# Kernel optimization log

Measured on AMD Instinct MI355X. Metric: run time of the kernel, lower is better.

Reference implementation:

```python
import jax, jax.numpy as jnp
import numpy as np

B, N, C, H, L, D_FF = 32, 196, 768, 12, 4, 3072

def _ln(x, g, b, eps=1e-6):
    m = x.mean(-1, keepdims=True)
    v = ((x - m) ** 2).mean(-1, keepdims=True)
    return (x - m) / jnp.sqrt(v + eps) * g + b

def _sdpa(q, k, v, scale):
    a = jax.nn.softmax(jnp.einsum('...qd,...kd->...qk', q, k) * scale, axis=-1)
    return jnp.einsum('...qk,...kd->...qd', a, v)

def _vit_attn(x, qkv_w, qkv_b, proj_w, proj_b):
    Bs, Ns, Cs = x.shape
    hd = Cs // H
    qkv = (x @ qkv_w + qkv_b).reshape(Bs, Ns, 3, H, hd).transpose(2, 0, 3, 1, 4)
    q, k, v = qkv[0], qkv[1], qkv[2]  # [B,H,N,hd]
    o = _sdpa(q, k, v, hd ** -0.5).transpose(0, 2, 1, 3).reshape(Bs, Ns, Cs)
    return o @ proj_w + proj_b

def _mlp(x, w1, b1, w2, b2):
    return jax.nn.gelu(x @ w1 + b1, approximate=False) @ w2 + b2

def setup_inputs() -> dict:
    key = jax.random.key(0)
    ks = jax.random.split(key, 16)
    w = lambda k, s: (jax.random.normal(k, s, jnp.float32) * 0.02)
    inp = {
        'x': jax.random.normal(ks[0], (B, N, C), jnp.float32),
        'y': jax.random.normal(ks[1], (B, N, C), jnp.float32),
        'latents': w(ks[2], (1, L, C)),
        'scale_a': jnp.zeros((1,), jnp.float32),
        'scale_v': jnp.zeros((1,), jnp.float32),
    }
    for i, p in enumerate(['s', 'r']):
        kk = jax.random.split(ks[3 + i], 4)
        inp.update({
            f'{p}_ln1_g': jnp.ones((C,), jnp.float32),
            f'{p}_ln1_b': jnp.zeros((C,), jnp.float32),
            f'{p}_qkv_w': w(kk[0], (C, 3 * C)),
            f'{p}_qkv_b': jnp.zeros((3 * C,), jnp.float32),
            f'{p}_proj_w': w(kk[1], (C, C)),
            f'{p}_proj_b': jnp.zeros((C,), jnp.float32),
            f'{p}_ln2_g': jnp.ones((C,), jnp.float32),
            f'{p}_ln2_b': jnp.zeros((C,), jnp.float32),
            f'{p}_fc1_w': w(kk[2], (C, D_FF)),
            f'{p}_fc1_b': jnp.zeros((D_FF,), jnp.float32),
            f'{p}_fc2_w': w(kk[3], (D_FF, C)),
            f'{p}_fc2_b': jnp.zeros((C,), jnp.float32),
        })
    return inp

def reference(x, y, latents, scale_a, scale_v,
              s_ln1_g, s_ln1_b, s_qkv_w, s_qkv_b, s_proj_w, s_proj_b,
              s_ln2_g, s_ln2_b, s_fc1_w, s_fc1_b, s_fc2_w, s_fc2_b,
              r_ln1_g, r_ln1_b, r_qkv_w, r_qkv_b, r_proj_w, r_proj_b,
              r_ln2_g, r_ln2_b, r_fc1_w, r_fc1_b, r_fc2_w, r_fc2_b):
    BS = x.shape[0]
    Cf = x.shape[-1]
    # --- latent bottleneck fusion (single-head, scale = C**-0.5) ---
    concat = jnp.concatenate([x, y], axis=1)            # [B, Na+Nv, C]
    lat = jnp.broadcast_to(latents, (BS,) + latents.shape[1:])
    fused = _sdpa(lat, concat, concat, Cf ** -0.5)      # [B, L, C]
    x = x + scale_a * _sdpa(x, fused, fused, Cf ** -0.5)
    y = y + scale_v * _sdpa(y, fused, fused, Cf ** -0.5)
    # --- standard ViT blocks per stream ---
    x = x + _vit_attn(_ln(x, s_ln1_g, s_ln1_b), s_qkv_w, s_qkv_b, s_proj_w, s_proj_b)
    y = y + _vit_attn(_ln(y, r_ln1_g, r_ln1_b), r_qkv_w, r_qkv_b, r_proj_w, r_proj_b)
    x = x + _mlp(_ln(x, s_ln2_g, s_ln2_b), s_fc1_w, s_fc1_b, s_fc2_w, s_fc2_b)
    y = y + _mlp(_ln(y, r_ln2_g, r_ln2_b), r_fc1_w, r_fc1_b, r_fc2_w, r_fc2_b)
    return (x, y)
```

## Files before the change

### kernel.cpp

```cpp
#include <hip/hip_runtime.h>
#include <hip/hip_bf16.h>
#include <math.h>

constexpr int Bc   = 32;
constexpr int Nc   = 196;
constexpr int Cc   = 768;
constexpr int Hc   = 12;
constexpr int HDc  = 64;
constexpr int Lc   = 4;
constexpr int DFFc = 3072;
constexpr int NCAT = 2 * Nc;
constexpr int Mrows = Bc * Nc;
constexpr float SCALE_C = 0.03608439182435161f;
constexpr float SCALE_H = 0.125f;
constexpr float LOG2E   = 1.4426950408889634f;

typedef __attribute__((ext_vector_type(8))) short short8;
typedef __attribute__((ext_vector_type(4))) short s16x4;
typedef __attribute__((ext_vector_type(4))) float float4a;
typedef __attribute__((ext_vector_type(4))) _Float16 half4;

__device__ inline float gelu_exact(float v) {
    return 0.5f * v * (1.0f + erff(v * 0.7071067811865476f));
}

__device__ inline void store_val(float* p, float v) { *p = v; }
__device__ inline void store_val(__hip_bfloat16* p, float v) { *p = __float2bfloat16(v); }

__device__ inline void gload16(const void* g, void* l) {
    __builtin_amdgcn_global_load_lds(
        (const __attribute__((address_space(1))) void*)g,
        (__attribute__((address_space(3))) void*)l, 16, 0, 0);
}

__global__ __launch_bounds__(256) void lat_scores_ker(
    const float* __restrict__ x, const float* __restrict__ y,
    const float* __restrict__ lat, float* __restrict__ scores)
{
    int wglobal = blockIdx.x * 4 + (threadIdx.x >> 6);
    int lane = threadIdx.x & 63;
    int b = wglobal / NCAT, j = wglobal % NCAT;
    const float* row = (j < Nc) ? x + ((size_t)b * Nc + j) * Cc
                                : y + ((size_t)b * Nc + (j - Nc)) * Cc;
    float a0 = 0.f, a1 = 0.f, a2 = 0.f, a3 = 0.f;
    for (int c = lane; c < Cc; c += 64) {
        float rv = row[c];
        a0 += rv * lat[c];
        a1 += rv * lat[Cc + c];
        a2 += rv * lat[2 * Cc + c];
        a3 += rv * lat[3 * Cc + c];
    }
    #pragma unroll
    for (int o = 32; o; o >>= 1) {
        a0 += __shfl_xor(a0, o);
        a1 += __shfl_xor(a1, o);
        a2 += __shfl_xor(a2, o);
        a3 += __shfl_xor(a3, o);
    }
    if (lane == 0) {
        float* sb = scores + (size_t)b * Lc * NCAT + j;
        sb[0 * NCAT] = a0 * SCALE_C;
        sb[1 * NCAT] = a1 * SCALE_C;
        sb[2 * NCAT] = a2 * SCALE_C;
        sb[3 * NCAT] = a3 * SCALE_C;
    }
}

__global__ __launch_bounds__(256) void lat_softmax_ker(float* __restrict__ scores)
{
    int b = blockIdx.x;
    int w = threadIdx.x >> 6, lane = threadIdx.x & 63;
    float* row = scores + (size_t)b * Lc * NCAT + w * NCAT;
    float m = -INFINITY;
    for (int j = lane; j < NCAT; j += 64) m = fmaxf(m, row[j]);
    #pragma unroll
    for (int o = 32; o; o >>= 1) m = fmaxf(m, __shfl_xor(m, o));
    float sum = 0.f;
    float e0 = expf(row[lane] - m);
    float e1 = expf(row[lane + 64] - m);
    float e2 = expf(row[lane + 128] - m);
    float e3 = expf(row[lane + 192] - m);
    float e4 = expf(row[lane + 256] - m);
    float e5 = expf(row[lane + 320] - m);
    float e6 = (lane < 8) ? expf(row[lane + 384] - m) : 0.f;
    sum = e0 + e1 + e2 + e3 + e4 + e5 + e6;
    #pragma unroll
    for (int o = 32; o; o >>= 1) sum += __shfl_xor(sum, o);
    float inv = 1.f / sum;
    row[lane] = e0 * inv;
    row[lane + 64] = e1 * inv;
    row[lane + 128] = e2 * inv;
    row[lane + 192] = e3 * inv;
    row[lane + 256] = e4 * inv;
    row[lane + 320] = e5 * inv;
    if (lane < 8) row[lane + 384] = e6 * inv;
}

__global__ __launch_bounds__(256) void lat_fused_ker(
    const float* __restrict__ x, const float* __restrict__ y,
    const float* __restrict__ probs, float* __restrict__ fused)
{
    int b = blockIdx.x, chunk = blockIdx.y;
    int t = threadIdx.x;
    int l = t >> 6;
    int c = chunk * 64 + (t & 63);
    __shared__ float p[Lc][NCAT];
    for (int idx = t; idx < Lc * NCAT; idx += 256)
        (&p[0][0])[idx] = probs[(size_t)b * Lc * NCAT + idx];
    __syncthreads();

    float acc0 = 0.f, acc1 = 0.f;
    for (int j = 0; j < Nc; j += 2) {
        const float* r0 = x + ((size_t)b * Nc + j) * Cc;
        acc0 += p[l][j] * r0[c];
        acc1 += p[l][j + 1] * r0[Cc + c];
    }
    for (int j = 0; j < Nc; j += 2) {
        const float* r0 = y + ((size_t)b * Nc + j) * Cc;
        acc0 += p[l][Nc + j] * r0[c];
        acc1 += p[l][Nc + j + 1] * r0[Cc + c];
    }
    fused[(size_t)b * Lc * Cc + l * Cc + c] = acc0 + acc1;
}

__global__ __launch_bounds__(256) void inject_ker(
    const float* __restrict__ x, const float* __restrict__ y,
    const float* __restrict__ fused,
    const float* __restrict__ scale_a, const float* __restrict__ scale_v,
    float* __restrict__ out)
{
    int gid = blockIdx.x;
    int st = gid / Mrows;
    int bn = gid % Mrows;
    int b = bn / Nc;
    const float* src = st ? y : x;
    float scale = st ? scale_v[0] : scale_a[0];
    float* dst = out + (size_t)st * Mrows * Cc;
    const float* f = fused + (size_t)b * Lc * Cc;
    const float* row = src + (size_t)bn * Cc;

    __shared__ float sc[4];
    int w = threadIdx.x >> 6, lane = threadIdx.x & 63;
    float partial = 0.f;
    for (int c = lane; c < Cc; c += 64) partial += row[c] * f[w * Cc + c];
    #pragma unroll
    for (int o = 32; o; o >>= 1) partial += __shfl_xor(partial, o);
    if (lane == 0) sc[w] = partial * SCALE_C;
    __syncthreads();

    float s0 = sc[0], s1 = sc[1], s2 = sc[2], s3 = sc[3];
    float m = fmaxf(fmaxf(s0, s1), fmaxf(s2, s3));
    float e0 = expf(s0 - m), e1 = expf(s1 - m), e2 = expf(s2 - m), e3 = expf(s3 - m);
    float inv = 1.f / (e0 + e1 + e2 + e3);
    e0 *= inv; e1 *= inv; e2 *= inv; e3 *= inv;

    for (int c = threadIdx.x; c < Cc; c += 256) {
        float v = e0 * f[c] + e1 * f[Cc + c] + e2 * f[2 * Cc + c] + e3 * f[3 * Cc + c];
        dst[(size_t)bn * Cc + c] = row[c] + scale * v;
    }
}

__global__ __launch_bounds__(256) void ln_ker(
    const float* __restrict__ in, size_t inz,
    const float* __restrict__ g0, const float* __restrict__ b0,
    const float* __restrict__ g1, const float* __restrict__ b1,
    __hip_bfloat16* __restrict__ out, size_t outz)
{
    int z = blockIdx.z;
    const float* g = z ? g1 : g0;
    const float* bb = z ? b1 : b0;
    in += (size_t)z * inz; out += (size_t)z * outz;

    int row = blockIdx.x;
    __shared__ float buf[Cc];
    __shared__ float red[4];
    __shared__ float red2[4];
    const float* r = in + (size_t)row * Cc;
    int w = threadIdx.x >> 6, lane = threadIdx.x & 63;

    float s = 0.f;
    for (int c = threadIdx.x; c < Cc; c += 256) {
        float v = r[c];
        buf[c] = v;
        s += v;
    }
    #pragma unroll
    for (int o = 32; o; o >>= 1) s += __shfl_xor(s, o);
    if (lane == 0) red[w] = s;
    __syncthreads();
    float mean = (red[0] + red[1] + red[2] + red[3]) * (1.f / Cc);

    float vs = 0.f;
    for (int c = threadIdx.x; c < Cc; c += 256) {
        float d = buf[c] - mean;
        vs += d * d;
    }
    #pragma unroll
    for (int o = 32; o; o >>= 1) vs += __shfl_xor(vs, o);
    if (lane == 0) red2[w] = vs;
    __syncthreads();
    float var = (red2[0] + red2[1] + red2[2] + red2[3]) * (1.f / Cc);
    float inv = 1.f / sqrtf(var + 1e-6f);

    for (int c = threadIdx.x; c < Cc; c += 256)
        out[(size_t)row * Cc + c] =
            __float2bfloat16((buf[c] - mean) * inv * g[c] + bb[c]);
}

struct WArgs {
    const float* src[8];
    __hip_bfloat16* dst[8];
};

__global__ __launch_bounds__(256) void wcast_all_ker(WArgs wa)
{
    int z = blockIdx.z;
    int bx = blockIdx.x;
    int which, tile, K_, N_;
    if (bx < 1728)      { which = 0; tile = bx;        K_ = 768;  N_ = 2304; }
    else if (bx < 2304) { which = 1; tile = bx - 1728; K_ = 768;  N_ = 768;  }
    else if (bx < 4608) { which = 2; tile = bx - 2304; K_ = 768;  N_ = 3072; }
    else                { which = 3; tile = bx - 4608; K_ = 3072; N_ = 768;  }
    const float* W = wa.src[z * 4 + which];
    __hip_bfloat16* WT = wa.dst[z * 4 + which];
    int ntx = N_ >> 5;
    int n0 = (tile % ntx) * 32, k0 = (tile / ntx) * 32;

    __shared__ float tilebuf[32][33];
    int t = threadIdx.x;
    int r = t >> 5, c = t & 31;
    #pragma unroll
    for (int p = 0; p < 4; ++p)
        tilebuf[r + p * 8][c] = W[(size_t)(k0 + r + p * 8) * N_ + n0 + c];
    __syncthreads();
    #pragma unroll
    for (int p = 0; p < 4; ++p)
        WT[(size_t)(n0 + r + p * 8) * K_ + k0 + c] =
            __float2bfloat16(tilebuf[c][r + p * 8]);
}

template <int EPI, typename OutT>
__global__ __launch_bounds__(256, 2) void gemm_bf16_ker(
    const __hip_bfloat16* __restrict__ A, size_t Az,
    const __hip_bfloat16* __restrict__ BT, size_t BTz,
    const float* __restrict__ bias0, const float* __restrict__ bias1,
    const float* __restrict__ res, size_t resz,
    OutT* __restrict__ out, size_t outz,
    int M_, int N_, int K_)
{
    const int z = blockIdx.z;
    A += (size_t)z * Az;
    BT += (size_t)z * BTz;
    const float* bias = z ? bias1 : bias0;
    res += (size_t)z * resz;
    out += (size_t)z * outz;

    __shared__ short As[128 * 32];
    __shared__ short Bs[128 * 32];
    const int t = threadIdx.x;
    const int wid = t >> 6, lane = t & 63;
    const int row0 = blockIdx.y * 128, col0 = blockIdx.x * 128;
    const int wr = (wid >> 1) * 64, wc = (wid & 1) * 64;

    const int f0 = wid * 1024 + lane * 16;
    const int f1 = f0 + 4096;
    const int r0s = f0 >> 6, r1s = f1 >> 6;
    const int u0 = ((f0 >> 4) & 3) ^ ((r0s >> 1) & 3);
    const int u1 = ((f1 >> 4) & 3) ^ ((r1s >> 1) & 3);

    const __hip_bfloat16* aS0 = A + (size_t)(row0 + r0s) * K_ + u0 * 8;
    const __hip_bfloat16* aS1 = A + (size_t)(row0 + r1s) * K_ + u1 * 8;
    const __hip_bfloat16* bS0 = BT + (size_t)(col0 + r0s) * K_ + u0 * 8;
    const __hip_bfloat16* bS1 = BT + (size_t)(col0 + r1s) * K_ + u1 * 8;
    short* ldsA0 = As + (wid * 1024) / 2;
    short* ldsA1 = As + (4096 + wid * 1024) / 2;
    short* ldsB0 = Bs + (wid * 1024) / 2;
    short* ldsB1 = Bs + (4096 + wid * 1024) / 2;

    const int fr = lane & 15;
    const int ku = lane >> 4;

    float4a acc[4][4];
    #pragma unroll
    for (int m = 0; m < 4; ++m)
        #pragma unroll
        for (int n = 0; n < 4; ++n)
            acc[m][n] = (float4a)0.f;

    for (int kt = 0; kt < K_; kt += 32) {
        gload16(aS0 + kt, ldsA0);
        gload16(aS1 + kt, ldsA1);
        gload16(bS0 + kt, ldsB0);
        gload16(bS1 + kt, ldsB1);
        __syncthreads();

        short8 af[4], bf[4];
        #pragma unroll
        for (int m = 0; m < 4; ++m) {
            int rl = wr + m * 16 + fr;
            int swz = ku ^ ((rl >> 1) & 3);
            af[m] = *(const short8*)(As + rl * 32 + swz * 8);
        }
        #pragma unroll
        for (int n = 0; n < 4; ++n) {
            int cl = wc + n * 16 + fr;
            int swz = ku ^ ((cl >> 1) & 3);
            bf[n] = *(const short8*)(Bs + cl * 32 + swz * 8);
        }
        #pragma unroll
        for (int m = 0; m < 4; ++m)
            #pragma unroll
            for (int n = 0; n < 4; ++n)
                acc[m][n] = __builtin_amdgcn_mfma_f32_16x16x32_bf16(
                    af[m], bf[n], acc[m][n], 0, 0, 0);
        __syncthreads();
    }

    const int fq = lane >> 4;
    #pragma unroll
    for (int m = 0; m < 4; ++m) {
        #pragma unroll
        for (int n = 0; n < 4; ++n) {
            int col = col0 + wc + n * 16 + fr;
            float b = bias[col];
            #pragma unroll
            for (int j = 0; j < 4; ++j) {
                int row = row0 + wr + m * 16 + fq * 4 + j;
                float v = acc[m][n][j] + b;
                if (EPI == 1) v = gelu_exact(v);
                if (EPI == 2) v += res[(size_t)row * N_ + col];
                store_val(out + (size_t)row * N_ + col, v);
            }
        }
    }
}

constexpr int NKT = 13;
constexpr int NQT = 13;
constexpr int NPAD = NKT * 16;
constexpr int VTS = 216;

__global__ __launch_bounds__(256) void attn_mfma_ker(
    const __hip_bfloat16* __restrict__ qkv, size_t qz,
    __hip_bfloat16* __restrict__ o, size_t oz)
{
    int z = blockIdx.z;
    qkv += (size_t)z * qz;
    o += (size_t)z * oz;

    int h = blockIdx.x, b = blockIdx.y;
    __shared__ short Ks[NPAD * 64];
    __shared__ _Float16 VT[64 * VTS];
    const size_t rs = 3 * Cc;
    const __hip_bfloat16* base = qkv + (size_t)b * Nc * rs + h * HDc;
    const int t = threadIdx.x;

    for (int c = t; c < NPAD * 8; c += 256) {
        int row = c >> 3, u = c & 7;
        int srow = row < Nc ? row : Nc - 1;
        short8 kv = *(const short8*)(base + (size_t)srow * rs + Cc + u * 8);
        *(short8*)(Ks + row * 64 + ((u ^ (row & 7)) << 3)) = kv;
        short8 vv = *(const short8*)(base + (size_t)srow * rs + 2 * Cc + u * 8);
        #pragma unroll
        for (int w = 0; w < 8; ++w) {
            __hip_bfloat16 bv = ((const __hip_bfloat16*)&vv)[w];
            VT[(u * 8 + w) * VTS + row] = (_Float16)__bfloat162float(bv);
        }
    }
    __syncthreads();

    const int wv = t >> 6, lane = t & 63;
    const int g = lane >> 4, c16 = lane & 15;
    const float KS = SCALE_H * LOG2E;

    for (int qt = wv; qt < NQT; qt += 4) {
        int qrow = qt * 16 + c16;
        int sq = qrow < Nc ? qrow : Nc - 1;
        const __hip_bfloat16* qb = base + (size_t)sq * rs + g * 8;
        short8 bq0 = *(const short8*)(qb);
        short8 bq1 = *(const short8*)(qb + 32);

        float4a acc[NKT];
        #pragma unroll
        for (int kt = 0; kt < NKT; ++kt) acc[kt] = (float4a)0.f;
        #pragma unroll
        for (int kt = 0; kt < NKT; ++kt) {
            int r = kt * 16 + c16;
            short8 a0 = *(const short8*)(Ks + r * 64 + ((g ^ (r & 7)) << 3));
            short8 a1 = *(const short8*)(Ks + r * 64 + (((4 + g) ^ (r & 7)) << 3));
            acc[kt] = __builtin_amdgcn_mfma_f32_16x16x32_bf16(a0, bq0, acc[kt], 0, 0, 0);
            acc[kt] = __builtin_amdgcn_mfma_f32_16x16x32_bf16(a1, bq1, acc[kt], 0, 0, 0);
        }

        float m = -INFINITY;
        #pragma unroll
        for (int kt = 0; kt < NKT; ++kt) {
            #pragma unroll
            for (int j = 0; j < 4; ++j) {
                int key = kt * 16 + g * 4 + j;
                float v = (key < Nc) ? acc[kt][j] * KS : -INFINITY;
                acc[kt][j] = v;
                m = fmaxf(m, v);
            }
        }
        m = fmaxf(m, __shfl_xor(m, 16));
        m = fmaxf(m, __shfl_xor(m, 32));

        float sum = 0.f;
        half4 pb[NKT];
        #pragma unroll
        for (int kt = 0; kt < NKT; ++kt) {
            #pragma unroll
            for (int j = 0; j < 4; ++j) {
                float e = exp2f(acc[kt][j] - m);
                sum += e;
                pb[kt][j] = (_Float16)e;
            }
        }
        sum += __shfl_xor(sum, 16);
        sum += __shfl_xor(sum, 32);
        float inv = 1.f / sum;

        float4a oa[4];
        #pragma unroll
        for (int dt = 0; dt < 4; ++dt) oa[dt] = (float4a)0.f;
        #pragma unroll
        for (int kt = 0; kt < NKT; ++kt) {
            #pragma unroll
            for (int dt = 0; dt < 4; ++dt) {
                half4 av = *(const half4*)(VT + (size_t)(dt * 16 + c16) * VTS
                                              + kt * 16 + g * 4);
                oa[dt] = __builtin_amdgcn_mfma_f32_16x16x16f16(av, pb[kt], oa[dt], 0, 0, 0);
            }
        }

        if (qrow < Nc) {
            __hip_bfloat16* ob = o + ((size_t)b * Nc + qrow) * Cc + h * HDc;
            #pragma unroll
            for (int dt = 0; dt < 4; ++dt) {
                __hip_bfloat16 tmp[4];
                #pragma unroll
                for (int j = 0; j < 4; ++j)
                    tmp[j] = __float2bfloat16(oa[dt][j] * inv);
                *(s16x4*)(ob + dt * 16 + g * 4) = *(const s16x4*)tmp;
            }
        }
    }
}

extern "C" void kernel_launch(void* const* d_in, const int* in_sizes, int n_in,
                              void* d_out, int out_size, void* d_ws, size_t ws_size,
                              hipStream_t stream)
{
    const float* x       = (const float*)d_in[0];
    const float* y       = (const float*)d_in[1];
    const float* latents = (const float*)d_in[2];
    const float* scale_a = (const float*)d_in[3];
    const float* scale_v = (const float*)d_in[4];

    float* out = (float*)d_out;

    constexpr size_t WSTREAM = 7077888;
    constexpr size_t OFF_QKV = 0;
    constexpr size_t OFF_PROJ = 2304 * 768;
    constexpr size_t OFF_FC1 = OFF_PROJ + 768 * 768;
    constexpr size_t OFF_FC2 = OFF_FC1 + 3072 * 768;

    constexpr size_t FRONT = ((size_t)Bc * Lc * NCAT + (size_t)Bc * Lc * Cc) * 4;
    constexpr size_t NEED_BATCH = FRONT
        + 2 * (size_t)Mrows * Cc * 2
        + 2 * (size_t)Mrows * DFFc * 2
        + 2 * WSTREAM * 2;

    float* ws = (float*)d_ws;
    float* scores = ws;
    float* fusedb = scores + (size_t)Bc * Lc * NCAT;

    const bool batched = ws_size >= NEED_BATCH;

    __hip_bfloat16* tbuf = (__hip_bfloat16*)(fusedb + (size_t)Bc * Lc * Cc);
    __hip_bfloat16* big;
    __hip_bfloat16* wT;
    if (batched) {
        big = tbuf + 2 * (size_t)Mrows * Cc;
        wT  = big + 2 * (size_t)Mrows * DFFc;
    } else {
        big = tbuf + (size_t)Mrows * Cc;
        wT  = big + (size_t)Mrows * DFFc;
    }

    lat_scores_ker<<<Bc * NCAT / 4, 256, 0, stream>>>(x, y, latents, scores);
    lat_softmax_ker<<<Bc, 256, 0, stream>>>(scores);
    lat_fused_ker<<<dim3(Bc, 12), 256, 0, stream>>>(x, y, scores, fusedb);
    inject_ker<<<2 * Mrows, 256, 0, stream>>>(x, y, fusedb, scale_a, scale_v, out);

    WArgs wa;
    for (int p = 0; p < 2; ++p) {
        int basei = 5 + 12 * p;
        wa.src[p * 4 + 0] = (const float*)d_in[basei + 2];
        wa.src[p * 4 + 1] = (const float*)d_in[basei + 4];
        wa.src[p * 4 + 2] = (const float*)d_in[basei + 8];
        wa.src[p * 4 + 3] = (const float*)d_in[basei + 10];
        wa.dst[p * 4 + 0] = wT + p * WSTREAM + OFF_QKV;
        wa.dst[p * 4 + 1] = wT + p * WSTREAM + OFF_PROJ;
        wa.dst[p * 4 + 2] = wT + p * WSTREAM + OFF_FC1;
        wa.dst[p * 4 + 3] = wT + p * WSTREAM + OFF_FC2;
    }
    wcast_all_ker<<<dim3(6912, 1, 2), 256, 0, stream>>>(wa);

    const float* g1[2], *b1[2], *qkvb[2], *projb[2], *g2[2], *b2[2], *fc1b[2], *fc2b[2];
    for (int p = 0; p < 2; ++p) {
        int basei = 5 + 12 * p;
        g1[p]    = (const float*)d_in[basei + 0];
        b1[p]    = (const float*)d_in[basei + 1];
        qkvb[p]  = (const float*)d_in[basei + 3];
        projb[p] = (const float*)d_in[basei + 5];
        g2[p]    = (const float*)d_in[basei + 6];
        b2[p]    = (const float*)d_in[basei + 7];
        fc1b[p]  = (const float*)d_in[basei + 9];
        fc2b[p]  = (const float*)d_in[basei + 11];
    }

    const size_t MC = (size_t)Mrows * Cc;
    const size_t MQKV = (size_t)Mrows * 2304;
    const size_t MFF = (size_t)Mrows * DFFc;

    if (batched) {
        ln_ker<<<dim3(Mrows, 1, 2), 256, 0, stream>>>(
            out, MC, g1[0], b1[0], g1[1], b1[1], tbuf, MC);
        gemm_bf16_ker<0, __hip_bfloat16><<<dim3(18, 49, 2), 256, 0, stream>>>(
            tbuf, MC, wT + OFF_QKV, WSTREAM, qkvb[0], qkvb[1],
            (const float*)out, 0, big, MQKV, Mrows, 2304, 768);
        attn_mfma_ker<<<dim3(Hc, Bc, 2), 256, 0, stream>>>(big, MQKV, tbuf, MC);
        gemm_bf16_ker<2, float><<<dim3(6, 49, 2), 256, 0, stream>>>(
            tbuf, MC, wT + OFF_PROJ, WSTREAM, projb[0], projb[1],
            (const float*)out, MC, out, MC, Mrows, 768, 768);
        ln_ker<<<dim3(Mrows, 1, 2), 256, 0, stream>>>(
            out, MC, g2[0], b2[0], g2[1], b2[1], tbuf, MC);
        gemm_bf16_ker<1, __hip_bfloat16><<<dim3(24, 49, 2), 256, 0, stream>>>(
            tbuf, MC, wT + OFF_FC1, WSTREAM, fc1b[0], fc1b[1],
            (const float*)out, 0, big, MFF, Mrows, 3072, 768);
        gemm_bf16_ker<2, float><<<dim3(6, 49, 2), 256, 0, stream>>>(
            big, MFF, wT + OFF_FC2, WSTREAM, fc2b[0], fc2b[1],
            (const float*)out, MC, out, MC, Mrows, 768, 3072);
    } else {
        for (int p = 0; p < 2; ++p) {
            float* X = out + (size_t)p * MC;
            __hip_bfloat16* wb = wT + p * WSTREAM;
            ln_ker<<<dim3(Mrows, 1, 1), 256, 0, stream>>>(
                X, 0, g1[p], b1[p], g1[p], b1[p], tbuf, 0);
            gemm_bf16_ker<0, __hip_bfloat16><<<dim3(18, 49, 1), 256, 0, stream>>>(
                tbuf, 0, wb + OFF_QKV, 0, qkvb[p], qkvb[p],
                (const float*)X, 0, big, 0, Mrows, 2304, 768);
            attn_mfma_ker<<<dim3(Hc, Bc, 1), 256, 0, stream>>>(big, 0, tbuf, 0);
            gemm_bf16_ker<2, float><<<dim3(6, 49, 1), 256, 0, stream>>>(
                tbuf, 0, wb + OFF_PROJ, 0, projb[p], projb[p],
                (const float*)X, 0, X, 0, Mrows, 768, 768);
            ln_ker<<<dim3(Mrows, 1, 1), 256, 0, stream>>>(
                X, 0, g2[p], b2[p], g2[p], b2[p], tbuf, 0);
            gemm_bf16_ker<1, __hip_bfloat16><<<dim3(24, 49, 1), 256, 0, stream>>>(
                tbuf, 0, wb + OFF_FC1, 0, fc1b[p], fc1b[p],
                (const float*)X, 0, big, 0, Mrows, 3072, 768);
            gemm_bf16_ker<2, float><<<dim3(6, 49, 1), 256, 0, stream>>>(
                big, 0, wb + OFF_FC2, 0, fc2b[p], fc2b[p],
                (const float*)X, 0, X, 0, Mrows, 768, 3072);
        }
    }
}
```

Baseline: 491.8 us.

## Fuse inject with LN1, add XCD-aware GEMM block remap, use tanh GELU

Merges the latent-injection kernel with the first LayerNorm so the residual stream is written once and normalized in the same pass, dropping one full read of the activations and a launch. The GEMM kernel remaps flat block indices so that consecutive tiles land on the same XCD, aiming for better L2 reuse. The exact erf GELU in the FC1 epilogue is replaced with the tanh approximation using a fast exp, which cuts epilogue cost but changes numerics relative to the exact reference.

Measured after the change: 442.4 us. -10.1%, faster.

```diff
diff --git a/kernel.cpp b/kernel.cpp
--- a/kernel.cpp
+++ b/kernel.cpp
@@ -20,8 +20,11 @@
 typedef __attribute__((ext_vector_type(4))) float float4a;
 typedef __attribute__((ext_vector_type(4))) _Float16 half4;
 
-__device__ inline float gelu_exact(float v) {
-    return 0.5f * v * (1.0f + erff(v * 0.7071067811865476f));
+__device__ inline float gelu_fast(float v) {
+    float c = v * (0.7978845608028654f + 0.035677408136300125f * v * v);
+    float ex = __expf(2.f * c);
+    float th = 1.f - 2.f / (ex + 1.f);
+    return 0.5f * v * (1.f + th);
 }
 
 __device__ inline void store_val(float* p, float v) { *p = v; }
@@ -160,6 +163,78 @@
     }
 }
 
+__global__ __launch_bounds__(256) void inject_ln_ker(
+    const float* __restrict__ x, const float* __restrict__ y,
+    const float* __restrict__ fusedb,
+    const float* __restrict__ scale_a, const float* __restrict__ scale_v,
+    const float* __restrict__ ga, const float* __restrict__ ba,
+    const float* __restrict__ gv, const float* __restrict__ bv,
+    float* __restrict__ out, __hip_bfloat16* __restrict__ lnout, size_t lnz)
+{
+    int gid = blockIdx.x;
+    int st = gid / Mrows;
+    int bn = gid % Mrows;
+    int b = bn / Nc;
+    const float* src = st ? y : x;
+    float scale = st ? scale_v[0] : scale_a[0];
+    const float* g  = st ? gv : ga;
+    const float* bb = st ? bv : ba;
+    float* dst = out + (size_t)st * Mrows * Cc + (size_t)bn * Cc;
+    __hip_bfloat16* lno = lnout + (size_t)st * lnz + (size_t)bn * Cc;
+    const float* f = fusedb + (size_t)b * Lc * Cc;
+    const float* row = src + (size_t)bn * Cc;
+
+    __shared__ float sc[4];
+    __shared__ float red[4];
+    int t = threadIdx.x;
+    int w = t >> 6, lane = t & 63;
+    float partial = 0.f;
+    for (int c = lane; c < Cc; c += 64) partial += row[c] * f[w * Cc + c];
+    #pragma unroll
+    for (int o = 32; o; o >>= 1) partial += __shfl_xor(partial, o);
+    if (lane == 0) sc[w] = partial * SCALE_C;
+    __syncthreads();
+
+    float s0 = sc[0], s1 = sc[1], s2 = sc[2], s3 = sc[3];
+    float m = fmaxf(fmaxf(s0, s1), fmaxf(s2, s3));
+    float e0 = expf(s0 - m), e1 = expf(s1 - m), e2 = expf(s2 - m), e3 = expf(s3 - m);
+    float inv = 1.f / (e0 + e1 + e2 + e3);
+    e0 *= inv; e1 *= inv; e2 *= inv; e3 *= inv;
+
+    float u[3];
+    float s = 0.f;
+    #pragma unroll
+    for (int k = 0; k < 3; ++k) {
+        int c = t + 256 * k;
+        float v = e0 * f[c] + e1 * f[Cc + c] + e2 * f[2 * Cc + c] + e3 * f[3 * Cc + c];
+        u[k] = row[c] + scale * v;
+        s += u[k];
+    }
+    #pragma unroll
+    for (int o = 32; o; o >>= 1) s += __shfl_xor(s, o);
+    if (lane == 0) red[w] = s;
+    __syncthreads();
+    float mean = (red[0] + red[1] + red[2] + red[3]) * (1.f / Cc);
+
+    float vs = 0.f;
+    #pragma unroll
+    for (int k = 0; k < 3; ++k) { float d = u[k] - mean; vs += d * d; }
+    #pragma unroll
+    for (int o = 32; o; o >>= 1) vs += __shfl_xor(vs, o);
+    __syncthreads();
+    if (lane == 0) red[w] = vs;
+    __syncthreads();
+    float var = (red[0] + red[1] + red[2] + red[3]) * (1.f / Cc);
+    float rinv = 1.f / sqrtf(var + 1e-6f);
+
+    #pragma unroll
+    for (int k = 0; k < 3; ++k) {
+        int c = t + 256 * k;
+        dst[c] = u[k];
+        lno[c] = __float2bfloat16((u[k] - mean) * rinv * g[c] + bb[c]);
+    }
+}
+
 __global__ __launch_bounds__(256) void ln_ker(
     const float* __restrict__ in, size_t inz,
     const float* __restrict__ g0, const float* __restrict__ b0,
@@ -248,7 +323,16 @@
     OutT* __restrict__ out, size_t outz,
     int M_, int N_, int K_)
 {
-    const int z = blockIdx.z;
+    const int gx = gridDim.x, gy = gridDim.y;
+    const long T = (long)gx * gy * gridDim.z;
+    long iflat = blockIdx.x + (long)gx * (blockIdx.y + (long)gy * blockIdx.z);
+    long q = T >> 3, r = T & 7;
+    long xcd = iflat & 7, jj = iflat >> 3;
+    long tt = (xcd < r ? xcd * (q + 1) : r * (q + 1) + (xcd - r) * q) + jj;
+    const int bx = (int)(tt % gx);
+    const int by = (int)((tt / gx) % gy);
+    const int z  = (int)(tt / ((long)gx * gy));
+
     A += (size_t)z * Az;
     BT += (size_t)z * BTz;
     const float* bias = z ? bias1 : bias0;
@@ -259,7 +343,7 @@
     __shared__ short Bs[128 * 32];
     const int t = threadIdx.x;
     const int wid = t >> 6, lane = t & 63;
-    const int row0 = blockIdx.y * 128, col0 = blockIdx.x * 128;
+    const int row0 = by * 128, col0 = bx * 128;
     const int wr = (wid >> 1) * 64, wc = (wid & 1) * 64;
 
     const int f0 = wid * 1024 + lane * 16;
@@ -294,7 +378,7 @@
         gload16(bS1 + kt, ldsB1);
         __syncthreads();
 
-        short8 af[4], bf[4];
+        short8 af[4], bf8[4];
         #pragma unroll
         for (int m = 0; m < 4; ++m) {
             int rl = wr + m * 16 + fr;
@@ -305,14 +389,14 @@
         for (int n = 0; n < 4; ++n) {
             int cl = wc + n * 16 + fr;
             int swz = ku ^ ((cl >> 1) & 3);
-            bf[n] = *(const short8*)(Bs + cl * 32 + swz * 8);
+            bf8[n] = *(const short8*)(Bs + cl * 32 + swz * 8);
         }
         #pragma unroll
         for (int m = 0; m < 4; ++m)
             #pragma unroll
             for (int n = 0; n < 4; ++n)
                 acc[m][n] = __builtin_amdgcn_mfma_f32_16x16x32_bf16(
-                    af[m], bf[n], acc[m][n], 0, 0, 0);
+                    af[m], bf8[n], acc[m][n], 0, 0, 0);
         __syncthreads();
     }
 
@@ -327,7 +411,7 @@
             for (int j = 0; j < 4; ++j) {
                 int row = row0 + wr + m * 16 + fq * 4 + j;
                 float v = acc[m][n][j] + b;
-                if (EPI == 1) v = gelu_exact(v);
+                if (EPI == 1) v = gelu_fast(v);
                 if (EPI == 2) v += res[(size_t)row * N_ + col];
                 store_val(out + (size_t)row * N_ + col, v);
             }
@@ -363,8 +447,8 @@
         short8 vv = *(const short8*)(base + (size_t)srow * rs + 2 * Cc + u * 8);
         #pragma unroll
         for (int w = 0; w < 8; ++w) {
-            __hip_bfloat16 bv = ((const __hip_bfloat16*)&vv)[w];
-            VT[(u * 8 + w) * VTS + row] = (_Float16)__bfloat162float(bv);
+            __hip_bfloat16 bvv = ((const __hip_bfloat16*)&vv)[w];
+            VT[(u * 8 + w) * VTS + row] = (_Float16)__bfloat162float(bvv);
         }
     }
     __syncthreads();
@@ -492,7 +576,6 @@
     lat_scores_ker<<<Bc * NCAT / 4, 256, 0, stream>>>(x, y, latents, scores);
     lat_softmax_ker<<<Bc, 256, 0, stream>>>(scores);
     lat_fused_ker<<<dim3(Bc, 12), 256, 0, stream>>>(x, y, scores, fusedb);
-    inject_ker<<<2 * Mrows, 256, 0, stream>>>(x, y, fusedb, scale_a, scale_v, out);
 
     WArgs wa;
     for (int p = 0; p < 2; ++p) {
@@ -506,7 +589,6 @@
         wa.dst[p * 4 + 2] = wT + p * WSTREAM + OFF_FC1;
         wa.dst[p * 4 + 3] = wT + p * WSTREAM + OFF_FC2;
     }
-    wcast_all_ker<<<dim3(6912, 1, 2), 256, 0, stream>>>(wa);
 
     const float* g1[2], *b1[2], *qkvb[2], *projb[2], *g2[2], *b2[2], *fc1b[2], *fc2b[2];
     for (int p = 0; p < 2; ++p) {
@@ -526,8 +608,10 @@
     const size_t MFF = (size_t)Mrows * DFFc;
 
     if (batched) {
-        ln_ker<<<dim3(Mrows, 1, 2), 256, 0, stream>>>(
-            out, MC, g1[0], b1[0], g1[1], b1[1], tbuf, MC);
+        inject_ln_ker<<<2 * Mrows, 256, 0, stream>>>(
+            x, y, fusedb, scale_a, scale_v,
+            g1[0], b1[0], g1[1], b1[1], out, tbuf, MC);
+        wcast_all_ker<<<dim3(6912, 1, 2), 256, 0, stream>>>(wa);
         gemm_bf16_ker<0, __hip_bfloat16><<<dim3(18, 49, 2), 256, 0, stream>>>(
             tbuf, MC, wT + OFF_QKV, WSTREAM, qkvb[0], qkvb[1],
             (const float*)out, 0, big, MQKV, Mrows, 2304, 768);
@@ -544,6 +628,8 @@
             big, MFF, wT + OFF_FC2, WSTREAM, fc2b[0], fc2b[1],
             (const float*)out, MC, out, MC, Mrows, 768, 3072);
     } else {
+        inject_ker<<<2 * Mrows, 256, 0, stream>>>(x, y, fusedb, scale_a, scale_v, out);
+        wcast_all_ker<<<dim3(6912, 1, 2), 256, 0, stream>>>(wa);
         for (int p = 0; p < 2; ++p) {
             float* X = out + (size_t)p * MC;
             __hip_bfloat16* wb = wT + p * WSTREAM;
```
